# Kernel tuning notes

Measured on AMD Instinct MI355X. Metric: run time of the kernel, lower is better.

## Reference

```python
import jax, jax.numpy as jnp
import numpy as np

N_NODES = 50000
N_EDGES = 800000
D_IN = 128
D_OUT = 128


def setup_inputs() -> dict:
    key = jax.random.key(0)
    k1, k2, k3, k4 = jax.random.split(key, 4)
    input_feature = jax.random.normal(k1, (N_NODES, D_IN), dtype=jnp.float32)
    # COO sparse adjacency: edge_index[0]=row (dst), edge_index[1]=col (src)
    edge_index = jax.random.randint(k2, (2, N_EDGES), 0, N_NODES, dtype=jnp.int32)
    edge_weight = jax.random.uniform(k3, (N_EDGES,), dtype=jnp.float32)
    # kaiming-uniform-like init for weight; zeros bias (as in reset_parameters)
    bound = float(np.sqrt(6.0 / D_IN))
    weight = jax.random.uniform(k4, (D_IN, D_OUT), dtype=jnp.float32, minval=-bound, maxval=bound)
    bias = jnp.zeros((D_OUT,), dtype=jnp.float32)
    return {
        "input_feature": input_feature,
        "edge_index": edge_index,
        "edge_weight": edge_weight,
        "weight": weight,
        "bias": bias,
    }


def reference(input_feature, edge_index, edge_weight, weight, bias):
    # support = X @ W  -> [N, D_OUT]
    support = input_feature @ weight
    # sparse A @ support via gather + weighted segment_sum over destination rows
    row, col = edge_index[0], edge_index[1]
    msgs = support[col] * edge_weight[:, None]          # [E, D_OUT]
    output = jax.ops.segment_sum(msgs, row, num_segments=N_NODES)
    return output + bias
```

## Files before the change

### kernel.cpp

```cpp
#include <hip/hip_runtime.h>


#define N_NODES 50000
#define N_EDGES 800000
#define D 128
#define BROWS 66
#define NBUCKET 758
#define SLOT 1536
#define CHUNK 4096
#define EPT 16
#define GEMM_BLOCKS 782
#define PASS1_BLOCKS 196
#define CSTRIDE 16

typedef short bf16x8 __attribute__((ext_vector_type(8)));
typedef float f32x4 __attribute__((ext_vector_type(4)));

__device__ inline unsigned short f2bf(float f) {
    unsigned u = __float_as_uint(f);
    unsigned r = (u + 0x7FFFu + ((u >> 16) & 1u)) >> 16;
    return (unsigned short)r;
}

__device__ inline void fma8(float* acc, uint4 v, float w) {
    acc[0] += __uint_as_float(v.x << 16) * w;
    acc[1] += __uint_as_float(v.x & 0xFFFF0000u) * w;
    acc[2] += __uint_as_float(v.y << 16) * w;
    acc[3] += __uint_as_float(v.y & 0xFFFF0000u) * w;
    acc[4] += __uint_as_float(v.z << 16) * w;
    acc[5] += __uint_as_float(v.z & 0xFFFF0000u) * w;
    acc[6] += __uint_as_float(v.w << 16) * w;
    acc[7] += __uint_as_float(v.w & 0xFFFF0000u) * w;
}


__global__ __launch_bounds__(256) void wprep_kernel(const float* __restrict__ W,
                                                    unsigned short* __restrict__ WT,
                                                    int* __restrict__ gcursor) {
    int idx = blockIdx.x * 256 + threadIdx.x;
    if (idx < 128 * 128) {
        int k = idx >> 7, n = idx & 127;
        WT[n * 136 + k] = f2bf(W[idx]);
    }
    if (idx < NBUCKET * CSTRIDE) gcursor[idx] = 0;
}

__global__ __launch_bounds__(256) void fused_kernel(const float* __restrict__ X,
                                                    const unsigned short* __restrict__ WT,
                                                    unsigned short* __restrict__ S16,
                                                    const int* __restrict__ ei,
                                                    const float* __restrict__ ew,
                                                    int* __restrict__ gcursor,
                                                    int2* __restrict__ staging) {
    __shared__ __align__(16) char shmem[52224];
    const int t = threadIdx.x;
    const int lane = t & 63, wid = t >> 6;

    if (blockIdx.x >= PASS1_BLOCKS) {
        unsigned short* wt = (unsigned short*)shmem;
        unsigned short* xt = (unsigned short*)(shmem + 34816);
        const int row0 = (blockIdx.x - PASS1_BLOCKS) * 64;

        const uint4* WTg = (const uint4*)WT;
        uint4* wl = (uint4*)wt;
#pragma unroll
        for (int i = 0; i < 9; ++i) {
            int idx = t + 256 * i;
            if (idx < 2176) wl[idx] = WTg[idx];
        }
        const float4* X4 = (const float4*)X;
#pragma unroll
        for (int i = 0; i < 8; ++i) {
            int idx4 = t + 256 * i;
            int r = idx4 >> 5, c4 = idx4 & 31;
            int gr = row0 + r;
            float4 v = make_float4(0.f, 0.f, 0.f, 0.f);
            if (gr < N_NODES) v = X4[gr * 32 + c4];
            ushort4 u = make_ushort4(f2bf(v.x), f2bf(v.y), f2bf(v.z), f2bf(v.w));
            *(ushort4*)&xt[r * 136 + c4 * 4] = u;
        }
        __syncthreads();

        const int m = lane & 15;
        const int q = lane >> 4;
        const int rbase = wid * 16;

        f32x4 acc[8];
#pragma unroll
        for (int nt = 0; nt < 8; ++nt) acc[nt] = (f32x4){0.f, 0.f, 0.f, 0.f};
#pragma unroll
        for (int ks = 0; ks < 4; ++ks) {
            bf16x8 a = *(const bf16x8*)&xt[(rbase + m) * 136 + ks * 32 + q * 8];
#pragma unroll
            for (int nt = 0; nt < 8; ++nt) {
                bf16x8 b = *(const bf16x8*)&wt[(nt * 16 + m) * 136 + ks * 32 + q * 8];
                acc[nt] = __builtin_amdgcn_mfma_f32_16x16x32_bf16(a, b, acc[nt], 0, 0, 0);
            }
        }
        __syncthreads();
#pragma unroll
        for (int nt = 0; nt < 8; ++nt) {
            int col = nt * 16 + m;
#pragma unroll
            for (int r = 0; r < 4; ++r) {
                int rl = rbase + q * 4 + r;
                xt[rl * 136 + col] = f2bf(acc[nt][r]);
            }
        }
        __syncthreads();
#pragma unroll
        for (int i = 0; i < 4; ++i) {
            int id = t + 256 * i;
            int r = id >> 4, c8 = (id & 15) * 8;
            int gr = row0 + r;
            if (gr < N_NODES)
                *(uint4*)&S16[gr * 128 + c8] = *(const uint4*)&xt[r * 136 + c8];
        }
    } else {
        int* bufx            = (int*)shmem;
        int* bufw            = (int*)(shmem + 16384);
        unsigned short* bof  = (unsigned short*)(shmem + 32768);
        int* hist            = (int*)(shmem + 40960);
        int* lcur            = (int*)(shmem + 44032);
        int* bmg             = (int*)(shmem + 47104);
        int* wsum            = (int*)(shmem + 50176);
        const int base = blockIdx.x * CHUNK;

        hist[t] = 0;
        hist[t + 256] = 0;
        hist[t + 512] = 0;
        __syncthreads();

        int rows[EPT];
        int bkt[EPT];
#pragma unroll
        for (int i = 0; i < EPT; ++i) {
            int e = base + t + 256 * i;
            rows[i] = (e < N_EDGES) ? ei[e] : -1;
            bkt[i] = (rows[i] >= 0) ? (rows[i] / BROWS) : -1;
            if (bkt[i] >= 0) atomicAdd(&hist[bkt[i]], 1);
        }
        __syncthreads();

        int run = 0, exv[3], vv[3];
#pragma unroll
        for (int ph = 0; ph < 3; ++ph) {
            int v = hist[ph * 256 + t];
            vv[ph] = v;
            int incl = v;
#pragma unroll
            for (int off = 1; off < 64; off <<= 1) {
                int x = __shfl_up(incl, off, 64);
                if (lane >= off) incl += x;
            }
            if (lane == 63) wsum[wid] = incl;
            __syncthreads();
            int pre = 0, tot = 0;
#pragma unroll
            for (int w = 0; w < 4; ++w) {
                int x = wsum[w];
                if (w < wid) pre += x;
                tot += x;
            }
            exv[ph] = run + incl - v + pre;
            run += tot;
            __syncthreads();
        }
        const int total = run;
        lcur[t] = exv[0];
        lcur[t + 256] = exv[1];
        lcur[t + 512] = exv[2];
#pragma unroll
        for (int ph = 0; ph < 3; ++ph) {
            int b = ph * 256 + t;
            if (b < NBUCKET) {
                int v = vv[ph];
                if (v > 0) {
                    int gb = atomicAdd(&gcursor[b * CSTRIDE], v);
                    bmg[b] = b * SLOT + gb - exv[ph];
                }
            }
        }
        __syncthreads();

#pragma unroll
        for (int i = 0; i < EPT; ++i) {
            if (rows[i] >= 0) {
                int e = base + t + 256 * i;
                int col = ei[N_EDGES + e];
                float w = ew[e];
                int b = bkt[i];
                int lp = atomicAdd(&lcur[b], 1);
                int lrow = rows[i] - b * BROWS;
                bufx[lp] = (int)(((unsigned)lrow << 16) | (unsigned)col);
                bufw[lp] = __float_as_int(w);
                bof[lp] = (unsigned short)b;
            }
        }
        __syncthreads();

        for (int lp = t; lp < total; lp += 256) {
            int b = bof[lp];
            int g = bmg[b] + lp;
            if (g < (b + 1) * SLOT)
                staging[g] = make_int2(bufx[lp], bufw[lp]);
        }
    }
}

__global__ __launch_bounds__(512) void sortgather_kernel(const unsigned short* __restrict__ S16,
                                                         const int* __restrict__ gcursor,
                                                         const int2* __restrict__ staging,
                                                         const float* __restrict__ bias,
                                                         float* __restrict__ out) {
    __shared__ int2 in0[SLOT];
    __shared__ int2 in1[SLOT];
    __shared__ int hist[128];
    __shared__ int exs[128];
    __shared__ int lcur[128];
    __shared__ int wsum[2];
    const int t = threadIdx.x;
    const int b = blockIdx.x;
    const int lane = t & 63;
    int cnt = gcursor[b * CSTRIDE];
    if (cnt > SLOT) cnt = SLOT;

    if (t < 128) hist[t] = 0;
    __syncthreads();

    for (int i = t; i < cnt; i += 512) {
        int2 v = staging[b * SLOT + i];
        in0[i] = v;
        atomicAdd(&hist[((unsigned)v.x >> 16) & 127u], 1);
    }
    __syncthreads();

    int v = 0, incl = 0;
    if (t < 128) {
        v = hist[t];
        incl = v;
#pragma unroll
        for (int off = 1; off < 64; off <<= 1) {
            int x = __shfl_up(incl, off, 64);
            if (lane >= off) incl += x;
        }
        if (lane == 63) wsum[t >> 6] = incl;
    }
    __syncthreads();
    if (t < 128) {
        int pre = (t >= 64) ? wsum[0] : 0;
        int ex = incl - v + pre;
        exs[t] = ex;
        lcur[t] = ex;
    }
    __syncthreads();

    for (int i = t; i < cnt; i += 512) {
        int2 e = in0[i];
        int lr = (int)(((unsigned)e.x >> 16) & 127u);
        int p = atomicAdd(&lcur[lr], 1);
        in1[p] = e;
    }
    __syncthreads();

    const int wv = t >> 6;
    const int sub = lane >> 4;
    const int q = lane & 15;
    const uint4* S4 = (const uint4*)S16;
    const float4* bias4 = (const float4*)bias;
    const float4 b0 = bias4[q * 2];
    const float4 b1 = bias4[q * 2 + 1];

    for (int rr = wv; rr < BROWS; rr += 8) {
        const int beg = exs[rr];
        const int end = beg + hist[rr];
        float acc[8];
#pragma unroll
        for (int i = 0; i < 8; ++i) acc[i] = 0.f;

        int p = beg + sub;
        for (; p + 4 < end; p += 8) {
            int2 cw0 = in1[p];
            int2 cw1 = in1[p + 4];
            uint4 v0 = S4[(cw0.x & 0xFFFF) * 16 + q];
            uint4 v1 = S4[(cw1.x & 0xFFFF) * 16 + q];
            float w0 = __int_as_float(cw0.y);
            float w1 = __int_as_float(cw1.y);
            fma8(acc, v0, w0);
            fma8(acc, v1, w1);
        }
        if (p < end) {
            int2 cw = in1[p];
            uint4 v2 = S4[(cw.x & 0xFFFF) * 16 + q];
            float w = __int_as_float(cw.y);
            fma8(acc, v2, w);
        }
#pragma unroll
        for (int i = 0; i < 8; ++i) acc[i] += __shfl_xor(acc[i], 16, 64);
#pragma unroll
        for (int i = 0; i < 8; ++i) acc[i] += __shfl_xor(acc[i], 32, 64);

        int gr = b * BROWS + rr;
        if (sub == 0 && gr < N_NODES) {
            float4 o0 = make_float4(acc[0] + b0.x, acc[1] + b0.y,
                                    acc[2] + b0.z, acc[3] + b0.w);
            float4 o1 = make_float4(acc[4] + b1.x, acc[5] + b1.y,
                                    acc[6] + b1.z, acc[7] + b1.w);
            ((float4*)out)[gr * 32 + q * 2] = o0;
            ((float4*)out)[gr * 32 + q * 2 + 1] = o1;
        }
    }
}

extern "C" void kernel_launch(void* const* d_in, const int* in_sizes, int n_in,
                              void* d_out, int out_size, void* d_ws, size_t ws_size,
                              hipStream_t stream) {
    const float* X    = (const float*)d_in[0];
    const int*   ei   = (const int*)d_in[1];
    const float* ew   = (const float*)d_in[2];
    const float* W    = (const float*)d_in[3];
    const float* bias = (const float*)d_in[4];
    float* out = (float*)d_out;

    char* ws = (char*)d_ws;
    unsigned short* S16 = (unsigned short*)(ws);
    int2* staging = (int2*)(ws + 12800000);
    int*  gcursor = (int*)(ws + 22114304);
    unsigned short* WT16 = (unsigned short*)(ws + 22162816);

    wprep_kernel<<<64, 256, 0, stream>>>(W, WT16, gcursor);
    fused_kernel<<<GEMM_BLOCKS + PASS1_BLOCKS, 256, 0, stream>>>(X, WT16, S16, ei, ew,
                                                                 gcursor, staging);
    sortgather_kernel<<<NBUCKET, 512, 0, stream>>>(S16, gcursor, staging, bias, out);
}
```

Measured before the change: 133.2 us.

## Shrink LDS footprint: halve bucketing chunk, read W from global, keep staging entries in registers

Halves the edges each bucketing block handles and doubles the number of bucketing blocks. The GEMM blocks now read the bf16 weight tile straight from global memory instead of first copying it into LDS. Together these cut the fused kernel's shared memory from about 52KB to about 30KB, which should let more blocks run per CU. In the sort-gather kernel, staged edges are held in registers across the histogram and scatter steps instead of an extra LDS array, which saves LDS and one pass. The cost is more global/L2 traffic for weight fragments and more registers per thread.

After: 136.3 us. 1.02x slower.

```diff
diff --git a/kernel.cpp b/kernel.cpp
--- a/kernel.cpp
+++ b/kernel.cpp
@@ -7,10 +7,10 @@
 #define BROWS 66
 #define NBUCKET 758
 #define SLOT 1536
-#define CHUNK 4096
-#define EPT 16
+#define CHUNK 2048
+#define EPT 8
 #define GEMM_BLOCKS 782
-#define PASS1_BLOCKS 196
+#define PASS1_BLOCKS 391
 #define CSTRIDE 16
 
 typedef short bf16x8 __attribute__((ext_vector_type(8)));
@@ -52,22 +52,14 @@
                                                     const float* __restrict__ ew,
                                                     int* __restrict__ gcursor,
                                                     int2* __restrict__ staging) {
-    __shared__ __align__(16) char shmem[52224];
+    __shared__ __align__(16) char shmem[29952];
     const int t = threadIdx.x;
     const int lane = t & 63, wid = t >> 6;
 
     if (blockIdx.x >= PASS1_BLOCKS) {
-        unsigned short* wt = (unsigned short*)shmem;
-        unsigned short* xt = (unsigned short*)(shmem + 34816);
+        unsigned short* xt = (unsigned short*)shmem;
         const int row0 = (blockIdx.x - PASS1_BLOCKS) * 64;
 
-        const uint4* WTg = (const uint4*)WT;
-        uint4* wl = (uint4*)wt;
-#pragma unroll
-        for (int i = 0; i < 9; ++i) {
-            int idx = t + 256 * i;
-            if (idx < 2176) wl[idx] = WTg[idx];
-        }
         const float4* X4 = (const float4*)X;
 #pragma unroll
         for (int i = 0; i < 8; ++i) {
@@ -93,7 +85,7 @@
             bf16x8 a = *(const bf16x8*)&xt[(rbase + m) * 136 + ks * 32 + q * 8];
 #pragma unroll
             for (int nt = 0; nt < 8; ++nt) {
-                bf16x8 b = *(const bf16x8*)&wt[(nt * 16 + m) * 136 + ks * 32 + q * 8];
+                bf16x8 b = *(const bf16x8*)&WT[(nt * 16 + m) * 136 + ks * 32 + q * 8];
                 acc[nt] = __builtin_amdgcn_mfma_f32_16x16x32_bf16(a, b, acc[nt], 0, 0, 0);
             }
         }
@@ -118,12 +110,12 @@
         }
     } else {
         int* bufx            = (int*)shmem;
-        int* bufw            = (int*)(shmem + 16384);
-        unsigned short* bof  = (unsigned short*)(shmem + 32768);
-        int* hist            = (int*)(shmem + 40960);
-        int* lcur            = (int*)(shmem + 44032);
-        int* bmg             = (int*)(shmem + 47104);
-        int* wsum            = (int*)(shmem + 50176);
+        int* bufw            = (int*)(shmem + 8192);
+        unsigned short* bof  = (unsigned short*)(shmem + 16384);
+        int* hist            = (int*)(shmem + 20480);
+        int* lcur            = (int*)(shmem + 23552);
+        int* bmg             = (int*)(shmem + 26624);
+        int* wsum            = (int*)(shmem + 29696);
         const int base = blockIdx.x * CHUNK;
 
         hist[t] = 0;
@@ -213,7 +205,6 @@
                                                          const int2* __restrict__ staging,
                                                          const float* __restrict__ bias,
                                                          float* __restrict__ out) {
-    __shared__ int2 in0[SLOT];
     __shared__ int2 in1[SLOT];
     __shared__ int hist[128];
     __shared__ int exs[128];
@@ -228,10 +219,22 @@
     if (t < 128) hist[t] = 0;
     __syncthreads();
 
-    for (int i = t; i < cnt; i += 512) {
-        int2 v = staging[b * SLOT + i];
-        in0[i] = v;
-        atomicAdd(&hist[((unsigned)v.x >> 16) & 127u], 1);
+    int2 e0, e1, e2;
+    int lr0 = -1, lr1 = -1, lr2 = -1;
+    if (t < cnt) {
+        e0 = staging[b * SLOT + t];
+        lr0 = (int)(((unsigned)e0.x >> 16) & 127u);
+        atomicAdd(&hist[lr0], 1);
+    }
+    if (t + 512 < cnt) {
+        e1 = staging[b * SLOT + t + 512];
+        lr1 = (int)(((unsigned)e1.x >> 16) & 127u);
+        atomicAdd(&hist[lr1], 1);
+    }
+    if (t + 1024 < cnt) {
+        e2 = staging[b * SLOT + t + 1024];
+        lr2 = (int)(((unsigned)e2.x >> 16) & 127u);
+        atomicAdd(&hist[lr2], 1);
     }
     __syncthreads();
 
@@ -255,12 +258,9 @@
     }
     __syncthreads();
 
-    for (int i = t; i < cnt; i += 512) {
-        int2 e = in0[i];
-        int lr = (int)(((unsigned)e.x >> 16) & 127u);
-        int p = atomicAdd(&lcur[lr], 1);
-        in1[p] = e;
-    }
+    if (lr0 >= 0) { int p = atomicAdd(&lcur[lr0], 1); in1[p] = e0; }
+    if (lr1 >= 0) { int p = atomicAdd(&lcur[lr1], 1); in1[p] = e1; }
+    if (lr2 >= 0) { int p = atomicAdd(&lcur[lr2], 1); in1[p] = e2; }
     __syncthreads();
 
     const int wv = t >> 6;
```

## Double fused kernel block size to 512 threads and restructure bucket scan

Applied to the files above, without the earlier changes.

Raises the fused GEMM/bucketing kernel from 256 to 512 threads per block. In the GEMM path each wave now computes half the output columns for its 16-row tile, and in the bucketing path each thread handles 8 edges instead of 16. The three-phase histogram prefix scan is replaced by a single scan over 512 buckets plus a partial scan over the rest, with fewer block barriers. This adds parallelism and shortens the serial scan per block, at the cost of larger blocks, which may lower occupancy given the 52 KB of shared memory.

Result: no change. 132.7 us (-0.4%).

```diff
diff --git a/kernel.cpp b/kernel.cpp
--- a/kernel.cpp
+++ b/kernel.cpp
@@ -8,7 +8,7 @@
 #define NBUCKET 758
 #define SLOT 1536
 #define CHUNK 4096
-#define EPT 16
+#define EPT 8
 #define GEMM_BLOCKS 782
 #define PASS1_BLOCKS 196
 #define CSTRIDE 16
@@ -45,7 +45,7 @@
     if (idx < NBUCKET * CSTRIDE) gcursor[idx] = 0;
 }
 
-__global__ __launch_bounds__(256) void fused_kernel(const float* __restrict__ X,
+__global__ __launch_bounds__(512) void fused_kernel(const float* __restrict__ X,
                                                     const unsigned short* __restrict__ WT,
                                                     unsigned short* __restrict__ S16,
                                                     const int* __restrict__ ei,
@@ -64,14 +64,14 @@
         const uint4* WTg = (const uint4*)WT;
         uint4* wl = (uint4*)wt;
 #pragma unroll
-        for (int i = 0; i < 9; ++i) {
-            int idx = t + 256 * i;
+        for (int i = 0; i < 5; ++i) {
+            int idx = t + 512 * i;
             if (idx < 2176) wl[idx] = WTg[idx];
         }
         const float4* X4 = (const float4*)X;
 #pragma unroll
-        for (int i = 0; i < 8; ++i) {
-            int idx4 = t + 256 * i;
+        for (int i = 0; i < 4; ++i) {
+            int idx4 = t + 512 * i;
             int r = idx4 >> 5, c4 = idx4 & 31;
             int gr = row0 + r;
             float4 v = make_float4(0.f, 0.f, 0.f, 0.f);
@@ -83,34 +83,36 @@
 
         const int m = lane & 15;
         const int q = lane >> 4;
-        const int rbase = wid * 16;
-
-        f32x4 acc[8];
-#pragma unroll
-        for (int nt = 0; nt < 8; ++nt) acc[nt] = (f32x4){0.f, 0.f, 0.f, 0.f};
+        const int rbase = (wid >> 1) * 16;
+        const int h = wid & 1;
+
+        f32x4 acc[4];
+#pragma unroll
+        for (int n4 = 0; n4 < 4; ++n4) acc[n4] = (f32x4){0.f, 0.f, 0.f, 0.f};
 #pragma unroll
         for (int ks = 0; ks < 4; ++ks) {
             bf16x8 a = *(const bf16x8*)&xt[(rbase + m) * 136 + ks * 32 + q * 8];
 #pragma unroll
-            for (int nt = 0; nt < 8; ++nt) {
+            for (int n4 = 0; n4 < 4; ++n4) {
+                int nt = h * 4 + n4;
                 bf16x8 b = *(const bf16x8*)&wt[(nt * 16 + m) * 136 + ks * 32 + q * 8];
-                acc[nt] = __builtin_amdgcn_mfma_f32_16x16x32_bf16(a, b, acc[nt], 0, 0, 0);
-            }
-        }
-        __syncthreads();
-#pragma unroll
-        for (int nt = 0; nt < 8; ++nt) {
-            int col = nt * 16 + m;
+                acc[n4] = __builtin_amdgcn_mfma_f32_16x16x32_bf16(a, b, acc[n4], 0, 0, 0);
+            }
+        }
+        __syncthreads();
+#pragma unroll
+        for (int n4 = 0; n4 < 4; ++n4) {
+            int col = (h * 4 + n4) * 16 + m;
 #pragma unroll
             for (int r = 0; r < 4; ++r) {
                 int rl = rbase + q * 4 + r;
-                xt[rl * 136 + col] = f2bf(acc[nt][r]);
-            }
-        }
-        __syncthreads();
-#pragma unroll
-        for (int i = 0; i < 4; ++i) {
-            int id = t + 256 * i;
+                xt[rl * 136 + col] = f2bf(acc[n4][r]);
+            }
+        }
+        __syncthreads();
+#pragma unroll
+        for (int i = 0; i < 2; ++i) {
+            int id = t + 512 * i;
             int r = id >> 4, c8 = (id & 15) * 8;
             int gr = row0 + r;
             if (gr < N_NODES)
@@ -124,61 +126,76 @@
         int* lcur            = (int*)(shmem + 44032);
         int* bmg             = (int*)(shmem + 47104);
         int* wsum            = (int*)(shmem + 50176);
+        int* wsum2           = (int*)(shmem + 50208);
         const int base = blockIdx.x * CHUNK;
 
         hist[t] = 0;
-        hist[t + 256] = 0;
-        hist[t + 512] = 0;
+        if (t < 256) hist[t + 512] = 0;
         __syncthreads();
 
         int rows[EPT];
         int bkt[EPT];
 #pragma unroll
         for (int i = 0; i < EPT; ++i) {
-            int e = base + t + 256 * i;
+            int e = base + t + 512 * i;
             rows[i] = (e < N_EDGES) ? ei[e] : -1;
             bkt[i] = (rows[i] >= 0) ? (rows[i] / BROWS) : -1;
             if (bkt[i] >= 0) atomicAdd(&hist[bkt[i]], 1);
         }
         __syncthreads();
 
-        int run = 0, exv[3], vv[3];
-#pragma unroll
-        for (int ph = 0; ph < 3; ++ph) {
-            int v = hist[ph * 256 + t];
-            vv[ph] = v;
-            int incl = v;
+        int v0 = hist[t];
+        int incl0 = v0;
+#pragma unroll
+        for (int off = 1; off < 64; off <<= 1) {
+            int x = __shfl_up(incl0, off, 64);
+            if (lane >= off) incl0 += x;
+        }
+        if (lane == 63) wsum[wid] = incl0;
+
+        int v1 = 0, incl1 = 0;
+        if (t < 256) {
+            v1 = hist[512 + t];
+            incl1 = v1;
 #pragma unroll
             for (int off = 1; off < 64; off <<= 1) {
-                int x = __shfl_up(incl, off, 64);
-                if (lane >= off) incl += x;
-            }
-            if (lane == 63) wsum[wid] = incl;
-            __syncthreads();
-            int pre = 0, tot = 0;
-#pragma unroll
-            for (int w = 0; w < 4; ++w) {
-                int x = wsum[w];
-                if (w < wid) pre += x;
-                tot += x;
-            }
-            exv[ph] = run + incl - v + pre;
-            run += tot;
-            __syncthreads();
-        }
-        const int total = run;
-        lcur[t] = exv[0];
-        lcur[t + 256] = exv[1];
-        lcur[t + 512] = exv[2];
-#pragma unroll
-        for (int ph = 0; ph < 3; ++ph) {
-            int b = ph * 256 + t;
-            if (b < NBUCKET) {
-                int v = vv[ph];
-                if (v > 0) {
-                    int gb = atomicAdd(&gcursor[b * CSTRIDE], v);
-                    bmg[b] = b * SLOT + gb - exv[ph];
-                }
+                int x = __shfl_up(incl1, off, 64);
+                if (lane >= off) incl1 += x;
+            }
+            if (lane == 63) wsum2[wid] = incl1;
+        }
+        __syncthreads();
+
+        int pre0 = 0, tot0 = 0;
+#pragma unroll
+        for (int w = 0; w < 8; ++w) {
+            int x = wsum[w];
+            if (w < wid) pre0 += x;
+            tot0 += x;
+        }
+        int tot1 = wsum2[0] + wsum2[1] + wsum2[2] + wsum2[3];
+        const int total = tot0 + tot1;
+        int ex0 = incl0 - v0 + pre0;
+        lcur[t] = ex0;
+        int ex1 = 0;
+        if (t < 256) {
+            int pre1 = 0;
+#pragma unroll
+            for (int w = 0; w < 4; ++w)
+                if (w < wid) pre1 += wsum2[w];
+            ex1 = tot0 + incl1 - v1 + pre1;
+            lcur[512 + t] = ex1;
+        }
+
+        if (v0 > 0) {
+            int gb = atomicAdd(&gcursor[t * CSTRIDE], v0);
+            bmg[t] = t * SLOT + gb - ex0;
+        }
+        if (t < 256) {
+            int b = 512 + t;
+            if (b < NBUCKET && v1 > 0) {
+                int gb = atomicAdd(&gcursor[b * CSTRIDE], v1);
+                bmg[b] = b * SLOT + gb - ex1;
             }
         }
         __syncthreads();
@@ -186,7 +203,7 @@
 #pragma unroll
         for (int i = 0; i < EPT; ++i) {
             if (rows[i] >= 0) {
-                int e = base + t + 256 * i;
+                int e = base + t + 512 * i;
                 int col = ei[N_EDGES + e];
                 float w = ew[e];
                 int b = bkt[i];
@@ -199,7 +216,7 @@
         }
         __syncthreads();
 
-        for (int lp = t; lp < total; lp += 256) {
+        for (int lp = t; lp < total; lp += 512) {
             int b = bof[lp];
             int g = bmg[b] + lp;
             if (g < (b + 1) * SLOT)
@@ -329,7 +346,7 @@
     unsigned short* WT16 = (unsigned short*)(ws + 22162816);
 
     wprep_kernel<<<64, 256, 0, stream>>>(W, WT16, gcursor);
-    fused_kernel<<<GEMM_BLOCKS + PASS1_BLOCKS, 256, 0, stream>>>(X, WT16, S16, ei, ew,
+    fused_kernel<<<GEMM_BLOCKS + PASS1_BLOCKS, 512, 0, stream>>>(X, WT16, S16, ei, ew,
                                                                  gcursor, staging);
     sortgather_kernel<<<NBUCKET, 512, 0, stream>>>(S16, gcursor, staging, bias, out);
 }
```
